# Performance work log

Measured on AMD Instinct MI355X. Metric: run time of the kernel, lower is better.

## Reference

```python
import jax, jax.numpy as jnp
import numpy as np

HIDDEN = 2048
NH = 16
NKV = 8
HD = 128
EPS = 1e-6
THETA = 10000.0
Q_SIZE = NH * HD
KV_SIZE = NKV * HD


def setup_inputs() -> dict:
    key = jax.random.key(0)
    k1, k2, k3, k4 = jax.random.split(key, 4)
    B, T = 2, 2048
    hidden_states = jax.random.normal(k1, (B, T, HIDDEN), dtype=jnp.float32)
    positions = jnp.broadcast_to(jnp.arange(T, dtype=jnp.int32)[None, :], (B, T))
    # learned params
    w_qkv = jax.random.normal(k2, (Q_SIZE + 2 * KV_SIZE, HIDDEN), dtype=jnp.float32) * (HIDDEN ** -0.5)
    w_o = jax.random.normal(k3, (HIDDEN, Q_SIZE), dtype=jnp.float32) * (Q_SIZE ** -0.5)
    rms_w = jnp.ones((HD,), dtype=jnp.float32) + 0.01 * jax.random.normal(k4, (HD,), dtype=jnp.float32)
    return {"positions": positions, "hidden_states": hidden_states,
            "w_qkv": w_qkv, "w_o": w_o, "rms_w": rms_w}


def _rms_norm(x, w):
    # per-head RMSNorm over last dim (head_dim)
    var = jnp.mean(jnp.square(x), axis=-1, keepdims=True)
    return x * jax.lax.rsqrt(var + EPS) * w


def _rope(positions, x):
    # NeoX-style rotary over full head_dim. positions: [B,T], x: [B,T,h,HD]
    half = HD // 2
    inv_freq = 1.0 / (THETA ** (jnp.arange(0, half, dtype=jnp.float32) / half))
    angles = positions.astype(jnp.float32)[..., None] * inv_freq  # [B,T,half]
    cos = jnp.cos(angles)[:, :, None, :]  # [B,T,1,half]
    sin = jnp.sin(angles)[:, :, None, :]
    x1, x2 = jnp.split(x, 2, axis=-1)
    return jnp.concatenate([x1 * cos - x2 * sin, x2 * cos + x1 * sin], axis=-1)


def reference(positions, hidden_states, w_qkv, w_o, rms_w):
    B, T, _ = hidden_states.shape
    qkv = jnp.einsum('bth,oh->bto', hidden_states, w_qkv)
    q = qkv[..., :Q_SIZE].reshape(B, T, NH, HD)
    k = qkv[..., Q_SIZE:Q_SIZE + KV_SIZE].reshape(B, T, NKV, HD)
    v = qkv[..., Q_SIZE + KV_SIZE:].reshape(B, T, NKV, HD)
    # QK-norm (qkv_bias=False path)
    q = _rms_norm(q, rms_w)
    k = _rms_norm(k, rms_w)
    q, k = _rope(positions, q), _rope(positions, k)
    # GQA attention, causal. group q heads onto kv heads: g = NH // NKV
    g = NH // NKV
    qg = q.reshape(B, T, NKV, g, HD)
    scale = HD ** -0.5
    scores = jnp.einsum('btkgd,bskd->bkgts', qg, k) * scale  # [B,NKV,g,T,T]
    causal = jnp.tril(jnp.ones((T, T), dtype=bool))
    scores = jnp.where(causal, scores, jnp.finfo(scores.dtype).min)
    probs = jax.nn.softmax(scores, axis=-1)
    o = jnp.einsum('bkgts,bskd->btkgd', probs, v).reshape(B, T, Q_SIZE)
    return jnp.einsum('bto,ho->bth', o, w_o)
```

## Files before the change

### kernel.cpp

```cpp
#include <hip/hip_runtime.h>
#include <hip/hip_bf16.h>

typedef __attribute__((ext_vector_type(8))) short short8;
typedef __attribute__((ext_vector_type(8))) unsigned short u16x8;
typedef __attribute__((ext_vector_type(4))) float f32x4;
typedef __attribute__((ext_vector_type(16))) float f32x16;

#define HIDDEN 2048
#define NH 16
#define NKV 8
#define HD 128
#define T_SEQ 2048
#define B_SZ 2
#define M_TOK (B_SZ * T_SEQ)
#define QSIZE (NH * HD)
#define KVSIZE (NKV * HD)
#define OUTQKV (QSIZE + 2 * KVSIZE)

__device__ __forceinline__ unsigned short f2bf(float f) {
  unsigned int u = __builtin_bit_cast(unsigned int, f);
  u += 0x7FFFu + ((u >> 16) & 1u);
  return (unsigned short)(u >> 16);
}
__device__ __forceinline__ float bf2f(unsigned short h) {
  return __builtin_bit_cast(float, (unsigned int)h << 16);
}

typedef __attribute__((address_space(3))) void lds_void;
typedef __attribute__((address_space(1))) const void glb_void;
__device__ __forceinline__ void gld16(const void* g, void* l) {
  __builtin_amdgcn_global_load_lds((glb_void*)g, (lds_void*)l, 16, 0, 0);
}

__device__ __forceinline__ float exp2fast(float x) {
  float r;
  asm("v_exp_f32 %0, %1" : "=v"(r) : "v"(x));
  return r;
}
__device__ __forceinline__ unsigned cvtpk(float lo, float hi) {
  unsigned r;
  asm("v_cvt_pk_bf16_f32 %0, %1, %2" : "=v"(r) : "v"(lo), "v"(hi));
  return r;
}
__device__ __forceinline__ void pl32swap(unsigned& a, unsigned& b) {
  asm volatile("v_permlane32_swap_b32 %0, %1" : "+v"(a), "+v"(b));
}

template <int N>
__device__ __forceinline__ void vwait();
template <> __device__ __forceinline__ void vwait<0>() { asm volatile("s_waitcnt vmcnt(0)" ::: "memory"); }
template <> __device__ __forceinline__ void vwait<4>() { asm volatile("s_waitcnt vmcnt(4)" ::: "memory"); }

#define SEG0 1048576
#define SEG1 1048576
#define SEG2 524288
#define SEG3 524288
__global__ __launch_bounds__(256) void prep_kernel(const float* __restrict__ hidden,
                                                   const float* __restrict__ w_qkv,
                                                   const float* __restrict__ w_o,
                                                   unsigned short* __restrict__ hb,
                                                   unsigned short* __restrict__ wqkvb,
                                                   unsigned short* __restrict__ wob,
                                                   float* __restrict__ outz) {
  size_t i = (size_t)blockIdx.x * blockDim.x + threadIdx.x;
  const float* src;
  unsigned short* dst;
  if (i < SEG0) { src = hidden; dst = hb; }
  else if (i < SEG0 + SEG1) { src = w_qkv; dst = wqkvb; i -= SEG0; }
  else if (i < SEG0 + SEG1 + SEG2) { src = w_o; dst = wob; i -= (SEG0 + SEG1); }
  else {
    i -= (SEG0 + SEG1 + SEG2);
    float4 z = {0.f, 0.f, 0.f, 0.f};
    float4* p = (float4*)outz + i * 4;
    p[0] = z; p[1] = z; p[2] = z; p[3] = z;
    return;
  }
  const float4* p = (const float4*)src + i * 2;
  float4 a = p[0], b = p[1];
  u16x8 o = {f2bf(a.x), f2bf(a.y), f2bf(a.z), f2bf(a.w),
             f2bf(b.x), f2bf(b.y), f2bf(b.z), f2bf(b.w)};
  ((u16x8*)dst)[i] = o;
}

template <bool ACC, typename TC>
__global__ __launch_bounds__(512, 2) void gemm8(const unsigned short* __restrict__ A,
                                                const unsigned short* __restrict__ B,
                                                TC* __restrict__ C,
                                                int M, int N, int K, int LDK) {
  __shared__ unsigned short lsA[4][8192];
  __shared__ unsigned short lsB[4][8192];
  const int tid = threadIdx.x;
  const int wave = tid >> 6, lane = tid & 63;
  const int wr = wave >> 2, wc = wave & 3;
  const int lr = lane & 15;
  const int ntn = N >> 8;
  const int ntiles = (M >> 8) * ntn;
  const int cpx = gridDim.x >> 3;
  const int wg = (blockIdx.x & 7) * cpx + (blockIdx.x >> 3);
  const int tile = wg % ntiles, kt = wg / ntiles;
  const int m0 = (tile / ntn) * 256, n0 = (tile % ntn) * 256;
  const int ce = 8 * ((lane >> 4) ^ ((lr >> 1) & 3));
  const int rr0 = tid >> 2;
  const int cle = 8 * ((tid & 3) ^ ((rr0 >> 1) & 3));
  const unsigned short* pA0 = A + (size_t)(m0 + rr0) * LDK + (size_t)kt * K + cle;
  const unsigned short* pA1 = pA0 + (size_t)128 * LDK;
  const unsigned short* pB0 = B + (size_t)(n0 + rr0) * LDK + (size_t)kt * K + cle;
  const unsigned short* pB1 = pB0 + (size_t)128 * LDK;
  const int dst0 = 8 * tid, dst1 = 4096 + 8 * tid;

  auto stageA = [&](int hn) {
    const int s = hn & 3;
    gld16(pA0 + hn * 32, &lsA[s][dst0]);
    gld16(pA1 + hn * 32, &lsA[s][dst1]);
  };
  auto stageB = [&](int hn) {
    const int s = hn & 3;
    gld16(pB0 + hn * 32, &lsB[s][dst0]);
    gld16(pB1 + hn * 32, &lsB[s][dst1]);
  };

  f32x4 acc[8][4] = {};
  short8 af[4], bfg[4];
  const int NT = K >> 6;

  stageA(0); stageB(0); stageA(1); stageB(1);
  vwait<0>();
  __syncthreads();

#define PHASE(KK, MH, STG, VM)                                                            \
  {                                                                                       \
    const int slot = sb + (KK);                                                           \
    _Pragma("unroll")                                                                     \
    for (int i = 0; i < 4; i++)                                                           \
      af[i] = *(const short8*)&lsA[slot][(wr * 128 + (MH)*64 + i * 16 + lr) * 32 + ce];   \
    if ((MH) == 0) {                                                                      \
      _Pragma("unroll")                                                                   \
      for (int j = 0; j < 4; j++)                                                         \
        bfg[j] = *(const short8*)&lsB[slot][(wc * 64 + j * 16 + lr) * 32 + ce];           \
    }                                                                                     \
    if (st) { STG; }                                                                      \
    if ((VM) == 1) {                                                                      \
      if (st) vwait<4>(); else vwait<0>();                                                \
    } else if ((VM) == 2) {                                                               \
      if (st) vwait<4>();                                                                 \
    }                                                                                     \
    __builtin_amdgcn_s_barrier();                                                         \
    __builtin_amdgcn_s_setprio(1);                                                        \
    _Pragma("unroll")                                                                     \
    for (int i = 0; i < 4; i++)                                                           \
      _Pragma("unroll")                                                                   \
      for (int j = 0; j < 4; j++)                                                         \
        acc[(MH)*4 + i][j] =                                                              \
            __builtin_amdgcn_mfma_f32_16x16x32_bf16(af[i], bfg[j], acc[(MH)*4 + i][j], 0, 0, 0); \
    __builtin_amdgcn_s_setprio(0);                                                        \
    __builtin_amdgcn_s_barrier();                                                         \
  }

  for (int t = 0; t < NT; t++) {
    const int sb = (2 * t) & 3;
    const bool st = (t < NT - 1);
    const int h2 = 2 * t + 2, h3 = 2 * t + 3;
    PHASE(0, 0, stageA(h2), 0)
    PHASE(0, 1, stageB(h2), 1)
    PHASE(1, 0, stageA(h3), 0)
    PHASE(1, 1, stageB(h3), 2)
  }
#undef PHASE

#pragma unroll
  for (int i = 0; i < 8; i++)
#pragma unroll
    for (int j = 0; j < 4; j++) {
      int gm = m0 + wr * 128 + i * 16 + (lane >> 4) * 4;
      int gn = n0 + wc * 64 + j * 16 + lr;
      TC* cp = C + (size_t)gm * N + gn;
#pragma unroll
      for (int r = 0; r < 4; r++) {
        if constexpr (ACC) unsafeAtomicAdd((float*)(cp + (size_t)r * N), acc[i][j][r]);
        else *(cp + (size_t)r * N) = (TC)f2bf(acc[i][j][r]);
      }
    }
}

__global__ void norm_rope_kernel(const unsigned short* __restrict__ qkv,
                                 const int* __restrict__ positions,
                                 const float* __restrict__ rms_w,
                                 unsigned short* __restrict__ qa,
                                 unsigned short* __restrict__ ka) {
  const int m = blockIdx.x;
  const int b = m >> 11, tt = m & 2047;
  const int lane = threadIdx.x;
  const float pos = (float)positions[m];
  const float inv_freq = powf(10000.0f, -(float)lane * (1.0f / 64.0f));
  float sv, cv;
  sincosf(pos * inv_freq, &sv, &cv);
  const float w1 = rms_w[lane], w2 = rms_w[lane + 64];
  const unsigned short* src = qkv + (size_t)m * OUTQKV;
  for (int h = 0; h < 24; h++) {
    unsigned short r1 = src[h * 128 + lane], r2 = src[h * 128 + 64 + lane];
    float x1 = bf2f(r1), x2 = bf2f(r2);
    float ss = x1 * x1 + x2 * x2;
    ss += __shfl_xor(ss, 1);  ss += __shfl_xor(ss, 2);  ss += __shfl_xor(ss, 4);
    ss += __shfl_xor(ss, 8);  ss += __shfl_xor(ss, 16); ss += __shfl_xor(ss, 32);
    float rstd = rsqrtf(ss * (1.0f / 128.0f) + 1e-6f);
    float y1 = x1 * rstd * w1, y2 = x2 * rstd * w2;
    float o1 = y1 * cv - y2 * sv, o2 = y2 * cv + y1 * sv;
    unsigned short* dst;
    if (h < 16) dst = qa + (((size_t)b * NH + h) * T_SEQ + tt) * HD;
    else        dst = ka + (((size_t)b * NKV + (h - 16)) * T_SEQ + tt) * HD;
    dst[lane] = f2bf(o1); dst[lane + 64] = f2bf(o2);
  }
}

__global__ __launch_bounds__(256) void v_transpose(const unsigned short* __restrict__ qkv,
                                                   unsigned short* __restrict__ vat) {
  __shared__ unsigned short tile[64][136];
  const int tt0 = blockIdx.x * 64;
  const int kvh = blockIdx.y, b = blockIdx.z;
  const int t = threadIdx.x;
  {
    const int tok = t >> 2, d0 = (t & 3) * 32;
    const unsigned short* src = qkv + (size_t)((size_t)b * T_SEQ + tt0 + tok) * OUTQKV
                                + QSIZE + KVSIZE + kvh * HD + d0;
#pragma unroll
    for (int i = 0; i < 4; i++)
      *(u16x8*)&tile[tok][d0 + i * 8] = *(const u16x8*)(src + i * 8);
  }
  __syncthreads();
  {
    const int d = t >> 1, c0 = (t & 1) * 32;
    unsigned short* dst = vat + ((size_t)((size_t)b * NKV + kvh) * HD + d) * T_SEQ + tt0 + c0;
#pragma unroll
    for (int j = 0; j < 4; j++) {
      u16x8 v;
#pragma unroll
      for (int e = 0; e < 8; e++) v[e] = tile[c0 + j * 8 + e][d];
      *(u16x8*)(dst + j * 8) = v;
    }
  }
}

__global__ __launch_bounds__(256, 2) void attn_kernel(const unsigned short* __restrict__ qa,
                                                      const unsigned short* __restrict__ ka,
                                                      const unsigned short* __restrict__ vat,
                                                      unsigned short* __restrict__ ob) {
  __shared__ unsigned short ks[2][64 * 128];
  __shared__ unsigned short vs[2][128 * 64];
  const int bx = blockIdx.x;
  const int qt = 31 - (bx >> 4);
  const int kvh = bx & 7, b = (bx >> 3) & 1;
  const int tid = threadIdx.x, w = tid >> 6, lane = tid & 63;
  const int l31 = lane & 31, h5 = lane >> 5;
  const int h = kvh * 2 + (w >> 1);
  const int qrow = qt * 64 + (w & 1) * 32 + l31;
  const float cexp = 0.08838834764831845f * 1.44269504088896340f;

  const unsigned short* Kg = ka + ((size_t)b * NKV + kvh) * T_SEQ * HD;
  const unsigned short* Vg = vat + ((size_t)b * NKV + kvh) * (size_t)HD * T_SEQ;

  short8 qf[8];
  {
    const unsigned short* Qg = qa + (((size_t)b * NH + h) * T_SEQ + qrow) * HD;
#pragma unroll
    for (int c = 0; c < 8; c++) qf[c] = *(const short8*)(Qg + c * 16 + h5 * 8);
  }

  auto stage = [&](int j, int buf) {
#pragma unroll
    for (int s = 0; s < 4; s++) {
      int g = s * 256 + tid;
      int kr = g >> 4;
      int kc = 8 * ((g & 15) ^ (kr & 15));
      gld16(Kg + (size_t)(j * 64 + kr) * HD + kc, &ks[buf][g * 8]);
    }
#pragma unroll
    for (int s = 0; s < 4; s++) {
      int g = s * 256 + tid;
      int vd = g >> 3;
      int vc = 8 * ((g & 7) ^ (vd & 7));
      gld16(Vg + (size_t)vd * T_SEQ + j * 64 + vc, &vs[buf][g * 8]);
    }
  };

  stage(0, 0);
  vwait<0>();
  __syncthreads();

  f32x16 oacc[4] = {};
  float mraw = -1e30f, m2 = -3.0e29f, lsum = 0.f;

  for (int j = 0; j <= qt; j++) {
    const int buf = j & 1;
    if (j < qt) stage(j + 1, buf ^ 1);

    f32x16 sacc[2] = {};
    __builtin_amdgcn_s_setprio(1);
#pragma unroll
    for (int c = 0; c < 8; c++) {
#pragma unroll
      for (int t = 0; t < 2; t++) {
        const int row = t * 32 + l31;
        short8 kf = *(const short8*)&ks[buf][row * 128 + ((c * 16 + h5 * 8) ^ (8 * (l31 & 15)))];
        sacc[t] = __builtin_amdgcn_mfma_f32_32x32x16_bf16(kf, qf[c], sacc[t], 0, 0, 0);
      }
    }
    __builtin_amdgcn_s_setprio(0);

    if (j * 64 + 63 > qt * 64 + (w & 1) * 32) {
#pragma unroll
      for (int t = 0; t < 2; t++)
#pragma unroll
        for (int r = 0; r < 16; r++) {
          int kvg = j * 64 + t * 32 + (r & 3) + 8 * (r >> 2) + 4 * h5;
          if (kvg > qrow) sacc[t][r] = -1e30f;
        }
    }
    float mx = sacc[0][0];
#pragma unroll
    for (int t = 0; t < 2; t++)
#pragma unroll
      for (int r = 0; r < 16; r++) mx = fmaxf(mx, sacc[t][r]);
    mx = fmaxf(mx, __shfl_xor(mx, 32));
    if (__any((mx - mraw) * cexp > 11.5f)) {
      float mn = fmaxf(mraw, mx);
      float corr = exp2fast((mraw - mn) * cexp);
      mraw = mn;
      m2 = mn * cexp;
      lsum *= corr;
#pragma unroll
      for (int dt = 0; dt < 4; dt++)
#pragma unroll
        for (int r = 0; r < 16; r++) oacc[dt][r] *= corr;
    }
    short8 pf[4];
#pragma unroll
    for (int kt = 0; kt < 4; kt++) {
      const int t = kt >> 1, r0 = (kt & 1) * 8;
      float e0 = exp2fast(sacc[t][r0 + 0] * cexp - m2);
      float e1 = exp2fast(sacc[t][r0 + 1] * cexp - m2);
      float e2 = exp2fast(sacc[t][r0 + 2] * cexp - m2);
      float e3 = exp2fast(sacc[t][r0 + 3] * cexp - m2);
      float e4 = exp2fast(sacc[t][r0 + 4] * cexp - m2);
      float e5 = exp2fast(sacc[t][r0 + 5] * cexp - m2);
      float e6 = exp2fast(sacc[t][r0 + 6] * cexp - m2);
      float e7 = exp2fast(sacc[t][r0 + 7] * cexp - m2);
      lsum += ((e0 + e1) + (e2 + e3)) + ((e4 + e5) + (e6 + e7));
      unsigned a0 = cvtpk(e0, e1), a1 = cvtpk(e2, e3);
      unsigned b0 = cvtpk(e4, e5), b1 = cvtpk(e6, e7);
      pl32swap(a0, b0);
      pl32swap(a1, b1);
      uint4 uu = make_uint4(a0, a1, b0, b1);
      pf[kt] = __builtin_bit_cast(short8, uu);
    }
    __builtin_amdgcn_s_setprio(1);
#pragma unroll
    for (int dt = 0; dt < 4; dt++) {
      const int d = dt * 32 + l31;
#pragma unroll
      for (int kt = 0; kt < 4; kt++) {
        short8 vf = *(const short8*)&vs[buf][d * 64 + ((kt * 16 + h5 * 8) ^ (8 * (l31 & 7)))];
        oacc[dt] = __builtin_amdgcn_mfma_f32_32x32x16_bf16(vf, pf[kt], oacc[dt], 0, 0, 0);
      }
    }
    __builtin_amdgcn_s_setprio(0);
    vwait<0>();
    __syncthreads();
  }

  lsum += __shfl_xor(lsum, 32);
  const float inv = 1.0f / lsum;
  unsigned short* dst = ob + ((size_t)b * T_SEQ + qrow) * QSIZE + h * HD;
#pragma unroll
  for (int dt = 0; dt < 4; dt++)
#pragma unroll
    for (int rg = 0; rg < 4; rg++) {
      ushort4 v4;
      v4.x = f2bf(oacc[dt][rg * 4 + 0] * inv);
      v4.y = f2bf(oacc[dt][rg * 4 + 1] * inv);
      v4.z = f2bf(oacc[dt][rg * 4 + 2] * inv);
      v4.w = f2bf(oacc[dt][rg * 4 + 3] * inv);
      *(ushort4*)(dst + dt * 32 + rg * 8 + 4 * h5) = v4;
    }
}

extern "C" void kernel_launch(void* const* d_in, const int* in_sizes, int n_in,
                              void* d_out, int out_size, void* d_ws, size_t ws_size,
                              hipStream_t stream) {
  const int* positions = (const int*)d_in[0];
  const float* hidden  = (const float*)d_in[1];
  const float* w_qkv   = (const float*)d_in[2];
  const float* w_o     = (const float*)d_in[3];
  const float* rms_w   = (const float*)d_in[4];
  float* out = (float*)d_out;

  unsigned short* qkv   = (unsigned short*)d_ws;
  unsigned short* hb    = qkv + (size_t)M_TOK * OUTQKV;
  unsigned short* wqkvb = hb + (size_t)M_TOK * HIDDEN;
  unsigned short* wob   = wqkvb + (size_t)OUTQKV * HIDDEN;
  unsigned short* qa    = hb;
  unsigned short* ka    = wqkvb;
  unsigned short* vat   = wqkvb + (size_t)B_SZ * NKV * T_SEQ * HD;
  unsigned short* ob    = qkv;

  const int prep_items = SEG0 + SEG1 + SEG2 + SEG3;
  prep_kernel<<<prep_items / 256, 256, 0, stream>>>(hidden, w_qkv, w_o, hb, wqkvb, wob, out);
  gemm8<false, unsigned short>
      <<<256, 512, 0, stream>>>(hb, wqkvb, qkv, M_TOK, OUTQKV, HIDDEN, HIDDEN);
  norm_rope_kernel<<<M_TOK, 64, 0, stream>>>(qkv, positions, rms_w, qa, ka);
  v_transpose<<<dim3(T_SEQ / 64, NKV, B_SZ), 256, 0, stream>>>(qkv, vat);
  attn_kernel<<<512, 256, 0, stream>>>(qa, ka, vat, ob);
  gemm8<true, float>
      <<<256, 512, 0, stream>>>(ob, wob, out, M_TOK, HIDDEN, QSIZE / 2, QSIZE);
}
```

Measured before the change: 257.8 us.

## Replace split-K atomics with partial buffer plus reduce, vectorize GEMM epilogue stores

The output GEMM no longer zeroes the output and atomically adds the two split-K halves. Each half now writes plain stores to either the output or a separate partial buffer, and a new reduce_add kernel sums them. The MFMA operands are swapped so each lane holds four consecutive columns, which lets the epilogue write 4-wide vector stores instead of scalar ones in both GEMMs. This costs an extra kernel launch and an extra pass over the output, and it needs workspace room for the fp32 partial buffer.

```diff
diff --git a/kernel.cpp b/kernel.cpp
--- a/kernel.cpp
+++ b/kernel.cpp
@@ -51,30 +51,31 @@
 template <> __device__ __forceinline__ void vwait<0>() { asm volatile("s_waitcnt vmcnt(0)" ::: "memory"); }
 template <> __device__ __forceinline__ void vwait<4>() { asm volatile("s_waitcnt vmcnt(4)" ::: "memory"); }
 
+__device__ __forceinline__ void store4(unsigned short* p, const f32x4& v) {
+  ushort4 o;
+  o.x = f2bf(v[0]); o.y = f2bf(v[1]); o.z = f2bf(v[2]); o.w = f2bf(v[3]);
+  *(ushort4*)p = o;
+}
+__device__ __forceinline__ void store4(float* p, const f32x4& v) {
+  float4 o = {v[0], v[1], v[2], v[3]};
+  *(float4*)p = o;
+}
+
 #define SEG0 1048576
 #define SEG1 1048576
 #define SEG2 524288
-#define SEG3 524288
 __global__ __launch_bounds__(256) void prep_kernel(const float* __restrict__ hidden,
                                                    const float* __restrict__ w_qkv,
                                                    const float* __restrict__ w_o,
                                                    unsigned short* __restrict__ hb,
                                                    unsigned short* __restrict__ wqkvb,
-                                                   unsigned short* __restrict__ wob,
-                                                   float* __restrict__ outz) {
+                                                   unsigned short* __restrict__ wob) {
   size_t i = (size_t)blockIdx.x * blockDim.x + threadIdx.x;
   const float* src;
   unsigned short* dst;
   if (i < SEG0) { src = hidden; dst = hb; }
   else if (i < SEG0 + SEG1) { src = w_qkv; dst = wqkvb; i -= SEG0; }
-  else if (i < SEG0 + SEG1 + SEG2) { src = w_o; dst = wob; i -= (SEG0 + SEG1); }
-  else {
-    i -= (SEG0 + SEG1 + SEG2);
-    float4 z = {0.f, 0.f, 0.f, 0.f};
-    float4* p = (float4*)outz + i * 4;
-    p[0] = z; p[1] = z; p[2] = z; p[3] = z;
-    return;
-  }
+  else { src = w_o; dst = wob; i -= (SEG0 + SEG1); }
   const float4* p = (const float4*)src + i * 2;
   float4 a = p[0], b = p[1];
   u16x8 o = {f2bf(a.x), f2bf(a.y), f2bf(a.z), f2bf(a.w),
@@ -82,10 +83,21 @@
   ((u16x8*)dst)[i] = o;
 }
 
-template <bool ACC, typename TC>
+__global__ __launch_bounds__(256) void reduce_add(float* __restrict__ out,
+                                                  const float* __restrict__ part, int n4) {
+  int stride = gridDim.x * blockDim.x;
+  for (int i = blockIdx.x * blockDim.x + threadIdx.x; i < n4; i += stride) {
+    float4 a = ((const float4*)out)[i];
+    float4 b = ((const float4*)part)[i];
+    a.x += b.x; a.y += b.y; a.z += b.z; a.w += b.w;
+    ((float4*)out)[i] = a;
+  }
+}
+
+template <typename TC>
 __global__ __launch_bounds__(512, 2) void gemm8(const unsigned short* __restrict__ A,
                                                 const unsigned short* __restrict__ B,
-                                                TC* __restrict__ C,
+                                                TC* __restrict__ C0, TC* __restrict__ C1,
                                                 int M, int N, int K, int LDK) {
   __shared__ unsigned short lsA[4][8192];
   __shared__ unsigned short lsB[4][8192];
@@ -151,7 +163,7 @@
       _Pragma("unroll")                                                                   \
       for (int j = 0; j < 4; j++)                                                         \
         acc[(MH)*4 + i][j] =                                                              \
-            __builtin_amdgcn_mfma_f32_16x16x32_bf16(af[i], bfg[j], acc[(MH)*4 + i][j], 0, 0, 0); \
+            __builtin_amdgcn_mfma_f32_16x16x32_bf16(bfg[j], af[i], acc[(MH)*4 + i][j], 0, 0, 0); \
     __builtin_amdgcn_s_setprio(0);                                                        \
     __builtin_amdgcn_s_barrier();                                                         \
   }
@@ -167,18 +179,14 @@
   }
 #undef PHASE
 
+  TC* Cw = (kt == 0) ? C0 : C1;
 #pragma unroll
   for (int i = 0; i < 8; i++)
 #pragma unroll
     for (int j = 0; j < 4; j++) {
-      int gm = m0 + wr * 128 + i * 16 + (lane >> 4) * 4;
-      int gn = n0 + wc * 64 + j * 16 + lr;
-      TC* cp = C + (size_t)gm * N + gn;
-#pragma unroll
-      for (int r = 0; r < 4; r++) {
-        if constexpr (ACC) unsafeAtomicAdd((float*)(cp + (size_t)r * N), acc[i][j][r]);
-        else *(cp + (size_t)r * N) = (TC)f2bf(acc[i][j][r]);
-      }
+      int gm = m0 + wr * 128 + i * 16 + lr;
+      int gn = n0 + wc * 64 + j * 16 + (lane >> 4) * 4;
+      store4(Cw + (size_t)gm * N + gn, acc[i][j]);
     }
 }
 
@@ -401,14 +409,16 @@
   unsigned short* ka    = wqkvb;
   unsigned short* vat   = wqkvb + (size_t)B_SZ * NKV * T_SEQ * HD;
   unsigned short* ob    = qkv;
-
-  const int prep_items = SEG0 + SEG1 + SEG2 + SEG3;
-  prep_kernel<<<prep_items / 256, 256, 0, stream>>>(hidden, w_qkv, w_o, hb, wqkvb, wob, out);
-  gemm8<false, unsigned short>
-      <<<256, 512, 0, stream>>>(hb, wqkvb, qkv, M_TOK, OUTQKV, HIDDEN, HIDDEN);
+  float* part = (float*)(qkv + (size_t)M_TOK * QSIZE);
+
+  const int prep_items = SEG0 + SEG1 + SEG2;
+  prep_kernel<<<prep_items / 256, 256, 0, stream>>>(hidden, w_qkv, w_o, hb, wqkvb, wob);
+  gemm8<unsigned short>
+      <<<256, 512, 0, stream>>>(hb, wqkvb, qkv, qkv, M_TOK, OUTQKV, HIDDEN, HIDDEN);
   norm_rope_kernel<<<M_TOK, 64, 0, stream>>>(qkv, positions, rms_w, qa, ka);
   v_transpose<<<dim3(T_SEQ / 64, NKV, B_SZ), 256, 0, stream>>>(qkv, vat);
   attn_kernel<<<512, 256, 0, stream>>>(qa, ka, vat, ob);
-  gemm8<true, float>
-      <<<256, 512, 0, stream>>>(ob, wob, out, M_TOK, HIDDEN, QSIZE / 2, QSIZE);
-}
+  gemm8<float>
+      <<<256, 512, 0, stream>>>(ob, wob, out, part, M_TOK, HIDDEN, QSIZE / 2, QSIZE);
+  reduce_add<<<2048, 256, 0, stream>>>(out, part, M_TOK * HIDDEN / 4);
+}
```

New measurement: 226.5 us. 1.14x faster.
